# Kernel tuning notes

Measured on AMD Instinct MI355X. Metric: run time of the kernel, lower is better.

Reference implementation:

```python
import jax, jax.numpy as jnp
import numpy as np

NUM_EXPERTS = 16
HIDDEN = 1024
INTERMEDIATE = 4096
TOTAL_TOKENS = 32768  # 2048 tokens per expert


def setup_inputs() -> dict:
    key = jax.random.key(0)
    k1, k2, k3 = jax.random.split(key, 3)
    hidden_states = jax.random.normal(k1, (TOTAL_TOKENS, HIDDEN), dtype=jnp.float32)
    gate_up_proj = jax.random.normal(k2, (NUM_EXPERTS, HIDDEN, 2 * INTERMEDIATE), dtype=jnp.float32)
    down_proj = jax.random.normal(k3, (NUM_EXPERTS, INTERMEDIATE, HIDDEN), dtype=jnp.float32)
    return {"hidden_states": hidden_states, "gate_up_proj": gate_up_proj, "down_proj": down_proj}


def reference(hidden_states, gate_up_proj, down_proj):
    E, H = gate_up_proj.shape[0], gate_up_proj.shape[1]
    # (E, T, H): tokens pre-grouped by expert, as in the torch module's reshape
    x = hidden_states.reshape(E, -1, H)
    # batched expert GEMM: (E,T,H) @ (E,H,2I) -> (E,T,2I)
    gate_up = jnp.einsum('eth,ehf->etf', x, gate_up_proj)
    gate, up = jnp.split(gate_up, 2, axis=-1)
    gated = up * jax.nn.silu(gate)  # SwiGLU
    # down projection: (E,T,I) @ (E,I,H) -> (E,T,H)
    out = jnp.einsum('eti,eih->eth', gated, down_proj)
    return out.reshape(-1, H)
```

## Files before the change

kernel.cpp:

```cpp
#include <hip/hip_runtime.h>
#include <hip/hip_bf16.h>
#include <cstdint>
#include <cstddef>

#define NE  16
#define HD  1024
#define ID  4096
#define TPE 2048
#define TOKENS 32768

typedef __attribute__((ext_vector_type(8))) short short8;
typedef __attribute__((ext_vector_type(4))) float f32x4;
typedef __attribute__((ext_vector_type(4))) unsigned short u16x4;
typedef __attribute__((ext_vector_type(8))) unsigned short u16x8;

static __device__ __forceinline__ unsigned short f2b(float f) {
    __bf16 h = (__bf16)f;
    return __builtin_bit_cast(unsigned short, h);
}

#define GLOAD16(gsrc, ldsbase)                                                  \
    __builtin_amdgcn_global_load_lds(                                           \
        (const __attribute__((address_space(1))) unsigned int*)(gsrc),          \
        (__attribute__((address_space(3))) unsigned int*)(ldsbase), 16, 0, 0)

#define MFMA16(a, b, c) __builtin_amdgcn_mfma_f32_16x16x32_bf16((a), (b), (c), 0, 0, 0)

__global__ void k_f2b(const float* __restrict__ src, unsigned short* __restrict__ dst, int n4)
{
    int i = blockIdx.x * blockDim.x + threadIdx.x;
    int stride = gridDim.x * blockDim.x;
    for (; i < n4; i += stride) {
        float4 v = *(const float4*)(src + (size_t)i * 4);
        u16x4 b = { f2b(v.x), f2b(v.y), f2b(v.z), f2b(v.w) };
        *(u16x4*)(dst + (size_t)i * 4) = b;
    }
}

__global__ __launch_bounds__(256) void k_transpose(const float* __restrict__ src,
                                                   unsigned short* __restrict__ dst,
                                                   int K, int N, int e0)
{
    __shared__ unsigned short LT[64][72];
    const int t  = threadIdx.x;
    const int eL = blockIdx.z;
    const float* s = src + (size_t)(e0 + eL) * K * N
                         + (size_t)(blockIdx.y * 64) * N + blockIdx.x * 64;
    unsigned short* d = dst + (size_t)eL * N * K
                            + (size_t)(blockIdx.x * 64) * K + blockIdx.y * 64;
    #pragma unroll
    for (int i = 0; i < 4; ++i) {
        int row = i * 16 + (t >> 4);
        int c4  = (t & 15) * 4;
        float4 v = *(const float4*)(s + (size_t)row * N + c4);
        LT[c4 + 0][row] = f2b(v.x);
        LT[c4 + 1][row] = f2b(v.y);
        LT[c4 + 2][row] = f2b(v.z);
        LT[c4 + 3][row] = f2b(v.w);
    }
    __syncthreads();
    #pragma unroll
    for (int i = 0; i < 2; ++i) {
        int n  = i * 32 + (t >> 3);
        int k8 = (t & 7) * 8;
        u16x8 v = *(const u16x8*)&LT[n][k8];
        *(u16x8*)(d + (size_t)n * K + k8) = v;
    }
}

__global__ __launch_bounds__(512, 2) void k_gemm1(const unsigned short* __restrict__ hsB,
                                                  const unsigned short* __restrict__ gupT,
                                                  unsigned short* __restrict__ gated,
                                                  int e0)
{
    __shared__ unsigned short As[2][256 * 64];
    __shared__ unsigned short Bs[2][256 * 64];
    const int NT = HD / 64;

    const int t    = threadIdx.x;
    const int lane = t & 63;
    const int w    = t >> 6;
    const int wr   = w >> 2;
    const int wc   = w & 3;
    const int eL   = blockIdx.z;
    const int e    = e0 + eL;
    const int n0g  = blockIdx.x * 128;
    const int m0   = blockIdx.y * 256;

    const unsigned short* gA  = hsB  + (size_t)(e * TPE + m0) * HD;
    const unsigned short* gBt = gupT + (size_t)eL * (2 * ID) * HD;

    f32x4 acc[8][4];
    #pragma unroll
    for (int i = 0; i < 8; ++i)
        #pragma unroll
        for (int j = 0; j < 4; ++j)
            acc[i][j] = f32x4{0.f, 0.f, 0.f, 0.f};

    auto STAGE = [&](int buf, int kt) {
        #pragma unroll
        for (int i = 0; i < 4; ++i) {
            int idx = i * 512 + t;
            int row = idx >> 3, sl = idx & 7;
            GLOAD16(gA + (size_t)row * HD + kt * 64 + ((sl ^ (row & 7)) << 3),
                    &As[buf][(size_t)(i * 512 + (t & ~63)) * 8]);
        }
        #pragma unroll
        for (int i = 0; i < 4; ++i) {
            int idx = i * 512 + t;
            int c = idx >> 3, sl = idx & 7;
            int g = c >> 5, j = c & 31;
            int grow = ((g & 1) ? ID : 0) + n0g + ((g >> 1) << 5) + j;
            GLOAD16(gBt + (size_t)grow * HD + kt * 64 + ((sl ^ (c & 7)) << 3),
                    &Bs[buf][(size_t)(i * 512 + (t & ~63)) * 8]);
        }
    };

    STAGE(0, 0);
    STAGE(1, 1);

    for (int kt = 0; kt < NT; ++kt) {
        const int cur = kt & 1;
        const unsigned short* Ab = &As[cur][0];
        const unsigned short* Bb = &Bs[cur][0];

        if (kt < NT - 1) { asm volatile("s_waitcnt vmcnt(8)" ::: "memory"); }
        else             { asm volatile("s_waitcnt vmcnt(0)" ::: "memory"); }
        __builtin_amdgcn_s_barrier();

        short8 av[8], bv[4];
        #pragma unroll
        for (int fm = 0; fm < 8; ++fm) {
            int row = wr * 128 + fm * 16 + (lane & 15);
            int sl  = (lane >> 4);
            av[fm] = *(const short8*)&Ab[row * 64 + ((sl ^ (row & 7)) << 3)];
        }
        #pragma unroll
        for (int fn = 0; fn < 4; ++fn) {
            int c  = wc * 64 + fn * 16 + (lane & 15);
            int sl = (lane >> 4);
            bv[fn] = *(const short8*)&Bb[c * 64 + ((sl ^ (c & 7)) << 3)];
        }
        __builtin_amdgcn_s_setprio(1);
        #pragma unroll
        for (int fm = 0; fm < 8; ++fm)
            #pragma unroll
            for (int fn = 0; fn < 4; ++fn)
                acc[fm][fn] = MFMA16(av[fm], bv[fn], acc[fm][fn]);
        __builtin_amdgcn_s_setprio(0);

        short8 av1[8], bv1[4];
        #pragma unroll
        for (int fm = 0; fm < 8; ++fm) {
            int row = wr * 128 + fm * 16 + (lane & 15);
            int sl  = 4 + (lane >> 4);
            av1[fm] = *(const short8*)&Ab[row * 64 + ((sl ^ (row & 7)) << 3)];
        }
        #pragma unroll
        for (int fn = 0; fn < 4; ++fn) {
            int c  = wc * 64 + fn * 16 + (lane & 15);
            int sl = 4 + (lane >> 4);
            bv1[fn] = *(const short8*)&Bb[c * 64 + ((sl ^ (c & 7)) << 3)];
        }
        asm volatile("s_waitcnt lgkmcnt(0)" ::: "memory");
        __builtin_amdgcn_sched_barrier(0);
        __builtin_amdgcn_s_barrier();
        if (kt + 2 < NT)
            STAGE(cur, kt + 2);
        __builtin_amdgcn_s_setprio(1);
        #pragma unroll
        for (int fm = 0; fm < 8; ++fm)
            #pragma unroll
            for (int fn = 0; fn < 4; ++fn)
                acc[fm][fn] = MFMA16(av1[fm], bv1[fn], acc[fm][fn]);
        __builtin_amdgcn_s_setprio(0);
    }

    unsigned short* g0 = gated + ((size_t)eL * TPE + m0) * ID;
    const int rq = (lane >> 4) << 2;
    const int cl = lane & 15;
    #pragma unroll
    for (int fm = 0; fm < 8; ++fm) {
        #pragma unroll
        for (int fp = 0; fp < 2; ++fp) {
            f32x4 g = acc[fm][fp];
            f32x4 u = acc[fm][fp + 2];
            #pragma unroll
            for (int r = 0; r < 4; ++r) {
                float gv  = g[r];
                float val = u[r] * gv / (1.0f + __expf(-gv));
                int row = wr * 128 + fm * 16 + rq + r;
                int col = n0g + wc * 32 + fp * 16 + cl;
                g0[(size_t)row * ID + col] = f2b(val);
            }
        }
    }
}

__global__ __launch_bounds__(512, 2) void k_gemm2(const unsigned short* __restrict__ gated,
                                                  const unsigned short* __restrict__ dwnT,
                                                  float* __restrict__ out,
                                                  int e0)
{
    __shared__ unsigned short As[2][256 * 64];
    __shared__ unsigned short Bs[2][256 * 64];
    const int NT = ID / 64;

    const int t    = threadIdx.x;
    const int lane = t & 63;
    const int w    = t >> 6;
    const int wr   = w >> 2;
    const int wc   = w & 3;
    const int eL   = blockIdx.z;
    const int e    = e0 + eL;
    const int n0   = blockIdx.x * 256;
    const int m0   = blockIdx.y * 256;

    const unsigned short* gA  = gated + ((size_t)eL * TPE + m0) * ID;
    const unsigned short* gBt = dwnT  + (size_t)eL * HD * ID;

    f32x4 acc[8][4];
    #pragma unroll
    for (int i = 0; i < 8; ++i)
        #pragma unroll
        for (int j = 0; j < 4; ++j)
            acc[i][j] = f32x4{0.f, 0.f, 0.f, 0.f};

    auto STAGE = [&](int buf, int kt) {
        #pragma unroll
        for (int i = 0; i < 4; ++i) {
            int idx = i * 512 + t;
            int row = idx >> 3, sl = idx & 7;
            GLOAD16(gA + (size_t)row * ID + kt * 64 + ((sl ^ (row & 7)) << 3),
                    &As[buf][(size_t)(i * 512 + (t & ~63)) * 8]);
        }
        #pragma unroll
        for (int i = 0; i < 4; ++i) {
            int idx = i * 512 + t;
            int c = idx >> 3, sl = idx & 7;
            GLOAD16(gBt + (size_t)(n0 + c) * ID + kt * 64 + ((sl ^ (c & 7)) << 3),
                    &Bs[buf][(size_t)(i * 512 + (t & ~63)) * 8]);
        }
    };

    STAGE(0, 0);
    STAGE(1, 1);

    for (int kt = 0; kt < NT; ++kt) {
        const int cur = kt & 1;
        const unsigned short* Ab = &As[cur][0];
        const unsigned short* Bb = &Bs[cur][0];

        if (kt < NT - 1) { asm volatile("s_waitcnt vmcnt(8)" ::: "memory"); }
        else             { asm volatile("s_waitcnt vmcnt(0)" ::: "memory"); }
        __builtin_amdgcn_s_barrier();

        short8 av[8], bv[4];
        #pragma unroll
        for (int fm = 0; fm < 8; ++fm) {
            int row = wr * 128 + fm * 16 + (lane & 15);
            int sl  = (lane >> 4);
            av[fm] = *(const short8*)&Ab[row * 64 + ((sl ^ (row & 7)) << 3)];
        }
        #pragma unroll
        for (int fn = 0; fn < 4; ++fn) {
            int c  = wc * 64 + fn * 16 + (lane & 15);
            int sl = (lane >> 4);
            bv[fn] = *(const short8*)&Bb[c * 64 + ((sl ^ (c & 7)) << 3)];
        }
        __builtin_amdgcn_s_setprio(1);
        #pragma unroll
        for (int fm = 0; fm < 8; ++fm)
            #pragma unroll
            for (int fn = 0; fn < 4; ++fn)
                acc[fm][fn] = MFMA16(av[fm], bv[fn], acc[fm][fn]);
        __builtin_amdgcn_s_setprio(0);

        short8 av1[8], bv1[4];
        #pragma unroll
        for (int fm = 0; fm < 8; ++fm) {
            int row = wr * 128 + fm * 16 + (lane & 15);
            int sl  = 4 + (lane >> 4);
            av1[fm] = *(const short8*)&Ab[row * 64 + ((sl ^ (row & 7)) << 3)];
        }
        #pragma unroll
        for (int fn = 0; fn < 4; ++fn) {
            int c  = wc * 64 + fn * 16 + (lane & 15);
            int sl = 4 + (lane >> 4);
            bv1[fn] = *(const short8*)&Bb[c * 64 + ((sl ^ (c & 7)) << 3)];
        }
        asm volatile("s_waitcnt lgkmcnt(0)" ::: "memory");
        __builtin_amdgcn_sched_barrier(0);
        __builtin_amdgcn_s_barrier();
        if (kt + 2 < NT)
            STAGE(cur, kt + 2);
        __builtin_amdgcn_s_setprio(1);
        #pragma unroll
        for (int fm = 0; fm < 8; ++fm)
            #pragma unroll
            for (int fn = 0; fn < 4; ++fn)
                acc[fm][fn] = MFMA16(av1[fm], bv1[fn], acc[fm][fn]);
        __builtin_amdgcn_s_setprio(0);
    }

    float* o0 = out + (size_t)(e * TPE + m0) * HD;
    const int rq = (lane >> 4) << 2;
    const int cl = lane & 15;
    #pragma unroll
    for (int fm = 0; fm < 8; ++fm) {
        #pragma unroll
        for (int fn = 0; fn < 4; ++fn) {
            #pragma unroll
            for (int r = 0; r < 4; ++r) {
                int row = wr * 128 + fm * 16 + rq + r;
                int col = n0 + wc * 64 + fn * 16 + cl;
                o0[(size_t)row * HD + col] = acc[fm][fn][r];
            }
        }
    }
}

extern "C" void kernel_launch(void* const* d_in, const int* in_sizes, int n_in,
                              void* d_out, int out_size, void* d_ws, size_t ws_size,
                              hipStream_t stream)
{
    (void)in_sizes; (void)n_in; (void)out_size;
    const float* hs  = (const float*)d_in[0];
    const float* gup = (const float*)d_in[1];
    const float* dwn = (const float*)d_in[2];
    float* out = (float*)d_out;

    const size_t SZ_HSB   = (size_t)TOKENS * HD * 2;
    const size_t SZ_GUPT  = (size_t)2 * ID * HD * 2;
    const size_t SZ_DWNT  = (size_t)HD * ID * 2;
    const size_t SZ_GATED = (size_t)TPE * ID * 2;
    const size_t perExp   = SZ_GUPT + SZ_DWNT + SZ_GATED;

    int G = (ws_size > SZ_HSB) ? (int)((ws_size - SZ_HSB) / perExp) : 1;
    if (G < 1) G = 1;
    if (G > NE) G = NE;

    unsigned short* hsB   = (unsigned short*)d_ws;
    unsigned short* gupT  = (unsigned short*)((char*)d_ws + SZ_HSB);
    unsigned short* dwnT  = (unsigned short*)((char*)d_ws + SZ_HSB + (size_t)G * SZ_GUPT);
    unsigned short* gated = (unsigned short*)((char*)d_ws + SZ_HSB + (size_t)G * (SZ_GUPT + SZ_DWNT));

    k_f2b<<<2048, 256, 0, stream>>>(hs, hsB, TOKENS * HD / 4);

    for (int e0 = 0; e0 < NE; e0 += G) {
        int ne = NE - e0;
        if (ne > G) ne = G;
        k_transpose<<<dim3((2 * ID) / 64, HD / 64, ne), 256, 0, stream>>>(gup, gupT, HD, 2 * ID, e0);
        k_transpose<<<dim3(HD / 64, ID / 64, ne), 256, 0, stream>>>(dwn, dwnT, ID, HD, e0);
        k_gemm1<<<dim3(ID / 128, TPE / 256, ne), 512, 0, stream>>>(hsB, gupT, gated, e0);
        k_gemm2<<<dim3(HD / 256, TPE / 256, ne), 512, 0, stream>>>(gated, dwnT, out, e0);
    }
}
```

Baseline: 1.150 ms.

## Swizzle GEMM workgroups across XCDs and vectorize transpose LDS writes

```diff
diff --git a/kernel.cpp b/kernel.cpp
--- a/kernel.cpp
+++ b/kernel.cpp
@@ -25,6 +25,11 @@
         (__attribute__((address_space(3))) unsigned int*)(ldsbase), 16, 0, 0)
 
 #define MFMA16(a, b, c) __builtin_amdgcn_mfma_f32_16x16x32_bf16((a), (b), (c), 0, 0, 0)
+
+static __device__ __forceinline__ int xcd_swz(int bid, int nwg) {
+    int q = nwg >> 3;
+    return (bid & 7) * q + (bid >> 3);
+}
 
 __global__ void k_f2b(const float* __restrict__ src, unsigned short* __restrict__ dst, int n4)
 {
@@ -48,15 +53,22 @@
                          + (size_t)(blockIdx.y * 64) * N + blockIdx.x * 64;
     unsigned short* d = dst + (size_t)eL * N * K
                             + (size_t)(blockIdx.x * 64) * K + blockIdx.y * 64;
-    #pragma unroll
-    for (int i = 0; i < 4; ++i) {
-        int row = i * 16 + (t >> 4);
-        int c4  = (t & 15) * 4;
-        float4 v = *(const float4*)(s + (size_t)row * N + c4);
-        LT[c4 + 0][row] = f2b(v.x);
-        LT[c4 + 1][row] = f2b(v.y);
-        LT[c4 + 2][row] = f2b(v.z);
-        LT[c4 + 3][row] = f2b(v.w);
+
+    const int ct = t & 15;
+    const int rt = t >> 4;
+    float4 v0 = *(const float4*)(s + (size_t)(rt * 4 + 0) * N + ct * 4);
+    float4 v1 = *(const float4*)(s + (size_t)(rt * 4 + 1) * N + ct * 4);
+    float4 v2 = *(const float4*)(s + (size_t)(rt * 4 + 2) * N + ct * 4);
+    float4 v3 = *(const float4*)(s + (size_t)(rt * 4 + 3) * N + ct * 4);
+    {
+        u16x4 w0 = { f2b(v0.x), f2b(v1.x), f2b(v2.x), f2b(v3.x) };
+        u16x4 w1 = { f2b(v0.y), f2b(v1.y), f2b(v2.y), f2b(v3.y) };
+        u16x4 w2 = { f2b(v0.z), f2b(v1.z), f2b(v2.z), f2b(v3.z) };
+        u16x4 w3 = { f2b(v0.w), f2b(v1.w), f2b(v2.w), f2b(v3.w) };
+        *(u16x4*)&LT[ct * 4 + 0][rt * 4] = w0;
+        *(u16x4*)&LT[ct * 4 + 1][rt * 4] = w1;
+        *(u16x4*)&LT[ct * 4 + 2][rt * 4] = w2;
+        *(u16x4*)&LT[ct * 4 + 3][rt * 4] = w3;
     }
     __syncthreads();
     #pragma unroll
@@ -77,15 +89,19 @@
     __shared__ unsigned short Bs[2][256 * 64];
     const int NT = HD / 64;
 
+    const int s    = xcd_swz(blockIdx.x, gridDim.x);
+    const int bx   = s & 31;
+    const int by   = (s >> 5) & 7;
+    const int eL   = s >> 8;
+
     const int t    = threadIdx.x;
     const int lane = t & 63;
     const int w    = t >> 6;
     const int wr   = w >> 2;
     const int wc   = w & 3;
-    const int eL   = blockIdx.z;
     const int e    = e0 + eL;
-    const int n0g  = blockIdx.x * 128;
-    const int m0   = blockIdx.y * 256;
+    const int n0g  = bx * 128;
+    const int m0   = by * 256;
 
     const unsigned short* gA  = hsB  + (size_t)(e * TPE + m0) * HD;
     const unsigned short* gBt = gupT + (size_t)eL * (2 * ID) * HD;
@@ -109,8 +125,8 @@
         for (int i = 0; i < 4; ++i) {
             int idx = i * 512 + t;
             int c = idx >> 3, sl = idx & 7;
-            int g = c >> 5, j = c & 31;
-            int grow = ((g & 1) ? ID : 0) + n0g + ((g >> 1) << 5) + j;
+            int g = c >> 5;
+            int grow = ((g & 1) ? ID : 0) + n0g + ((g >> 1) << 5) + (c & 31);
             GLOAD16(gBt + (size_t)grow * HD + kt * 64 + ((sl ^ (c & 7)) << 3),
                     &Bs[buf][(size_t)(i * 512 + (t & ~63)) * 8]);
         }
@@ -175,6 +191,7 @@
                 acc[fm][fn] = MFMA16(av1[fm], bv1[fn], acc[fm][fn]);
         __builtin_amdgcn_s_setprio(0);
     }
+    asm volatile("s_waitcnt vmcnt(0)" ::: "memory");
 
     unsigned short* g0 = gated + ((size_t)eL * TPE + m0) * ID;
     const int rq = (lane >> 4) << 2;
@@ -206,15 +223,19 @@
     __shared__ unsigned short Bs[2][256 * 64];
     const int NT = ID / 64;
 
+    const int s    = xcd_swz(blockIdx.x, gridDim.x);
+    const int bx   = s & 3;
+    const int by   = (s >> 2) & 7;
+    const int eL   = s >> 5;
+
     const int t    = threadIdx.x;
     const int lane = t & 63;
     const int w    = t >> 6;
     const int wr   = w >> 2;
     const int wc   = w & 3;
-    const int eL   = blockIdx.z;
     const int e    = e0 + eL;
-    const int n0   = blockIdx.x * 256;
-    const int m0   = blockIdx.y * 256;
+    const int n0   = bx * 256;
+    const int m0   = by * 256;
 
     const unsigned short* gA  = gated + ((size_t)eL * TPE + m0) * ID;
     const unsigned short* gBt = dwnT  + (size_t)eL * HD * ID;
@@ -302,6 +323,7 @@
                 acc[fm][fn] = MFMA16(av1[fm], bv1[fn], acc[fm][fn]);
         __builtin_amdgcn_s_setprio(0);
     }
+    asm volatile("s_waitcnt vmcnt(0)" ::: "memory");
 
     float* o0 = out + (size_t)(e * TPE + m0) * HD;
     const int rq = (lane >> 4) << 2;
@@ -352,7 +374,7 @@
         if (ne > G) ne = G;
         k_transpose<<<dim3((2 * ID) / 64, HD / 64, ne), 256, 0, stream>>>(gup, gupT, HD, 2 * ID, e0);
         k_transpose<<<dim3(HD / 64, ID / 64, ne), 256, 0, stream>>>(dwn, dwnT, ID, HD, e0);
-        k_gemm1<<<dim3(ID / 128, TPE / 256, ne), 512, 0, stream>>>(hsB, gupT, gated, e0);
-        k_gemm2<<<dim3(HD / 256, TPE / 256, ne), 512, 0, stream>>>(gated, dwnT, out, e0);
-    }
-}
+        k_gemm1<<<256 * ne, 512, 0, stream>>>(hsB, gupT, gated, e0);
+        k_gemm2<<<32 * ne, 512, 0, stream>>>(gated, dwnT, out, e0);
+    }
+}
```

After: 1.155 ms. No clear change (+0.5%).
